# Performance work log

Hardware: AMD Instinct MI355X
Metric: run time of the kernel (lower is better)

Reference implementation:

```python
import jax, jax.numpy as jnp
import numpy as np

L, D, H, T, B, V, R = 12, 1024, 16, 1024, 2, 50257, 32
HD = D // H
LORA_SCALE = 64.0 / 32.0  # alpha / rank
EPS = 1e-5


def setup_inputs() -> dict:
    key = jax.random.key(0)
    ks = iter(jax.random.split(key, 32))
    f = lambda shape, s=0.02: jax.random.normal(next(ks), shape, dtype=jnp.float32) * s
    inp = {
        'input_ids': jax.random.randint(next(ks), (B, T), 0, V, dtype=jnp.int64),
        'wte': f((V, D)), 'wpe': f((T, D)),
        'ln1_w': jnp.ones((L, D), jnp.float32), 'ln1_b': jnp.zeros((L, D), jnp.float32),
        'attn_w': f((L, 3 * D, D)), 'attn_b': jnp.zeros((L, 3 * D), jnp.float32),
        'attn_la': f((L, R, D), 0.01), 'attn_lb': f((L, 3 * D, R), 0.01),
        'proj_w': f((L, D, D)), 'proj_b': jnp.zeros((L, D), jnp.float32),
        'proj_la': f((L, R, D), 0.01), 'proj_lb': f((L, D, R), 0.01),
        'ln2_w': jnp.ones((L, D), jnp.float32), 'ln2_b': jnp.zeros((L, D), jnp.float32),
        'fc_w': f((L, 4 * D, D)), 'fc_b': jnp.zeros((L, 4 * D), jnp.float32),
        'fc_la': f((L, R, D), 0.01), 'fc_lb': f((L, 4 * D, R), 0.01),
        'mp_w': f((L, D, 4 * D)), 'mp_b': jnp.zeros((L, D), jnp.float32),
        'mp_la': f((L, R, 4 * D), 0.01), 'mp_lb': f((L, D, R), 0.01),
        'lnf_w': jnp.ones((D,), jnp.float32), 'lnf_b': jnp.zeros((D,), jnp.float32),
    }
    return inp


def _ln(x, w, b):
    m = jnp.mean(x, axis=-1, keepdims=True)
    v = jnp.mean(jnp.square(x - m), axis=-1, keepdims=True)
    return (x - m) * jax.lax.rsqrt(v + EPS) * w + b


def _lin(x, W, b, A, Bm):
    # quantized linear at 32-bit (pass-through) + LoRA: x W^T + b + scale * (x A^T) B^T
    return x @ W.T + b + ((x @ A.T) @ Bm.T) * LORA_SCALE


def _forward(input_ids, wte, wpe, ln1_w, ln1_b, attn_w, attn_b, attn_la, attn_lb,
             proj_w, proj_b, proj_la, proj_lb, ln2_w, ln2_b, fc_w, fc_b, fc_la, fc_lb,
             mp_w, mp_b, mp_la, mp_lb, lnf_w, lnf_b):
    Bq, Tq = input_ids.shape
    mask = jnp.tril(jnp.ones((Tq, Tq), dtype=bool))  # causal bias buffer
    h = wte[input_ids] + wpe[jnp.arange(Tq)]  # embed + (eval-mode) dropout

    def blk(h, p):
        l1w, l1b, aw, ab, ala, alb, pw, pb, pla, plb, l2w, l2b, fw, fb, fla, flb, mw, mb, mla, mlb = p
        x = _ln(h, l1w, l1b)
        qkv = _lin(x, aw, ab, ala, alb)  # [B,T,3D]
        q, k, v = jnp.split(qkv, 3, axis=-1)
        q = q.reshape(Bq, Tq, H, HD).transpose(0, 2, 1, 3)
        k = k.reshape(Bq, Tq, H, HD).transpose(0, 2, 1, 3)
        v = v.reshape(Bq, Tq, H, HD).transpose(0, 2, 1, 3)
        s = jnp.einsum('bhqd,bhkd->bhqk', q, k) / jnp.sqrt(jnp.float32(HD))
        s = jnp.where(mask, s, -jnp.inf)
        pa = jax.nn.softmax(s, axis=-1)
        o = jnp.einsum('bhqk,bhkd->bhqd', pa, v).transpose(0, 2, 1, 3).reshape(Bq, Tq, D)
        h = h + _lin(o, pw, pb, pla, plb)
        x = _ln(h, l2w, l2b)
        m = jax.nn.gelu(_lin(x, fw, fb, fla, flb), approximate=False)
        h = h + _lin(m, mw, mb, mla, mlb)
        return h, None

    h, _ = jax.lax.scan(blk, h, (ln1_w, ln1_b, attn_w, attn_b, attn_la, attn_lb,
                                 proj_w, proj_b, proj_la, proj_lb, ln2_w, ln2_b,
                                 fc_w, fc_b, fc_la, fc_lb, mp_w, mp_b, mp_la, mp_lb))
    return _ln(h, lnf_w, lnf_b)


def reference(input_ids, wte, wpe, ln1_w, ln1_b, attn_w, attn_b, attn_la, attn_lb,
              proj_w, proj_b, proj_la, proj_lb, ln2_w, ln2_b, fc_w, fc_b, fc_la, fc_lb,
              mp_w, mp_b, mp_la, mp_lb, lnf_w, lnf_b):
    return _forward(input_ids, wte, wpe, ln1_w, ln1_b, attn_w, attn_b, attn_la, attn_lb,
                    proj_w, proj_b, proj_la, proj_lb, ln2_w, ln2_b, fc_w, fc_b, fc_la, fc_lb,
                    mp_w, mp_b, mp_la, mp_lb, lnf_w, lnf_b)
```

## Files before the change

### kernel.cpp

```cpp
#include <hip/hip_runtime.h>
#include <math.h>

#define TT 1024
#define DD 1024
#define NH 16
#define NB 2
#define NL 12
#define RR 32
#define MM (NB * TT)

typedef __attribute__((ext_vector_type(8))) short bf16x8;
typedef __attribute__((ext_vector_type(4))) float f32x4;

__device__ __forceinline__ unsigned short f2bf(float f) {
  unsigned int u = __float_as_uint(f);
  u = (u + 0x7FFFu + ((u >> 16) & 1u)) >> 16;
  return (unsigned short)u;
}
__device__ __forceinline__ float bf2f(unsigned short u) {
  return __uint_as_float((unsigned int)u << 16);
}

typedef __attribute__((address_space(1))) void gvoid;
typedef __attribute__((address_space(3))) void lvoid;
__device__ __forceinline__ void gload_lds16(const void* g, void* l) {
  __builtin_amdgcn_global_load_lds((gvoid*)g, (lvoid*)l, 16, 0, 0);
}

__global__ __launch_bounds__(256) void embed_cvt_k(
    const int* __restrict__ ids, const float* __restrict__ wte,
    const float* __restrict__ wpe, float* __restrict__ h,
    const float* __restrict__ ala, const float* __restrict__ alb,
    const float* __restrict__ pla, const float* __restrict__ plb,
    const float* __restrict__ fla, const float* __restrict__ flb,
    const float* __restrict__ mla, const float* __restrict__ mlb,
    unsigned short* __restrict__ out) {
  if (blockIdx.x < MM * DD / 256) {
    const int i = blockIdx.x * 256 + threadIdx.x;
    const int row = i >> 10;
    const int d = i & 1023;
    const int t = row & (TT - 1);
    const int id = ids[row];
    h[i] = wte[(size_t)id * DD + d] + wpe[(size_t)t * DD + d];
    return;
  }
  const int g = (blockIdx.x - MM * DD / 256) * 256 + threadIdx.x;
  const int layer = g >> 19;
  const int rem = g & 524287;
  const int row = rem >> 5;
  const int r = rem & 31;
  float v;
  if (row < 1024)       v = ala[(size_t)layer * 32 * 1024 + r * 1024 + row];
  else if (row < 4096)  v = alb[(size_t)layer * 3072 * 32 + (row - 1024) * 32 + r];
  else if (row < 5120)  v = pla[(size_t)layer * 32 * 1024 + r * 1024 + (row - 4096)];
  else if (row < 6144)  v = plb[(size_t)layer * 1024 * 32 + (row - 5120) * 32 + r];
  else if (row < 7168)  v = fla[(size_t)layer * 32 * 1024 + r * 1024 + (row - 6144)];
  else if (row < 11264) v = flb[(size_t)layer * 4096 * 32 + (row - 7168) * 32 + r];
  else if (row < 15360) v = mla[(size_t)layer * 32 * 4096 + r * 4096 + (row - 11264)];
  else                  v = mlb[(size_t)layer * 1024 * 32 + (row - 15360) * 32 + r];
  out[g] = f2bf(v);
}

__global__ __launch_bounds__(256) void ln_bf_k(const float* __restrict__ x,
                                               const float* __restrict__ w,
                                               const float* __restrict__ b,
                                               unsigned short* __restrict__ out) {
  const int row = blockIdx.x;
  const float* xr = x + (size_t)row * DD;
  const float4 v = *(const float4*)(xr + threadIdx.x * 4);
  float s = v.x + v.y + v.z + v.w;
  float ss = v.x * v.x + v.y * v.y + v.z * v.z + v.w * v.w;
#pragma unroll
  for (int off = 32; off > 0; off >>= 1) {
    s += __shfl_down(s, off);
    ss += __shfl_down(ss, off);
  }
  __shared__ float rs[4], rss[4];
  const int wid = threadIdx.x >> 6;
  if ((threadIdx.x & 63) == 0) { rs[wid] = s; rss[wid] = ss; }
  __syncthreads();
  s = rs[0] + rs[1] + rs[2] + rs[3];
  ss = rss[0] + rss[1] + rss[2] + rss[3];
  const float mean = s * (1.f / DD);
  const float var = ss * (1.f / DD) - mean * mean;
  const float rstd = rsqrtf(var + 1e-5f);
  const float4 wv = *(const float4*)(w + threadIdx.x * 4);
  const float4 bv = *(const float4*)(b + threadIdx.x * 4);
  ushort4 o;
  o.x = f2bf((v.x - mean) * rstd * wv.x + bv.x);
  o.y = f2bf((v.y - mean) * rstd * wv.y + bv.y);
  o.z = f2bf((v.z - mean) * rstd * wv.z + bv.z);
  o.w = f2bf((v.w - mean) * rstd * wv.w + bv.w);
  *(ushort4*)(out + (size_t)row * DD + threadIdx.x * 4) = o;
}

__global__ __launch_bounds__(256) void ln_f_k(const float* __restrict__ x,
                                              const float* __restrict__ w,
                                              const float* __restrict__ b,
                                              float* __restrict__ out) {
  const int row = blockIdx.x;
  const float* xr = x + (size_t)row * DD;
  const float4 v = *(const float4*)(xr + threadIdx.x * 4);
  float s = v.x + v.y + v.z + v.w;
  float ss = v.x * v.x + v.y * v.y + v.z * v.z + v.w * v.w;
#pragma unroll
  for (int off = 32; off > 0; off >>= 1) {
    s += __shfl_down(s, off);
    ss += __shfl_down(ss, off);
  }
  __shared__ float rs[4], rss[4];
  const int wid = threadIdx.x >> 6;
  if ((threadIdx.x & 63) == 0) { rs[wid] = s; rss[wid] = ss; }
  __syncthreads();
  s = rs[0] + rs[1] + rs[2] + rs[3];
  ss = rss[4 - 4] + rss[1] + rss[2] + rss[3];
  const float mean = s * (1.f / DD);
  const float var = ss * (1.f / DD) - mean * mean;
  const float rstd = rsqrtf(var + 1e-5f);
  const float4 wv = *(const float4*)(w + threadIdx.x * 4);
  const float4 bv = *(const float4*)(b + threadIdx.x * 4);
  float4 o;
  o.x = (v.x - mean) * rstd * wv.x + bv.x;
  o.y = (v.y - mean) * rstd * wv.y + bv.y;
  o.z = (v.z - mean) * rstd * wv.z + bv.z;
  o.w = (v.w - mean) * rstd * wv.w + bv.w;
  *(float4*)(out + (size_t)row * DD + threadIdx.x * 4) = o;
}

__global__ __launch_bounds__(256) void fold_ln_k(
    const float* __restrict__ aw, const float* __restrict__ pw,
    const float* __restrict__ fw, const float* __restrict__ mw,
    const unsigned short* __restrict__ Lb,
    unsigned short* __restrict__ oq, unsigned short* __restrict__ op_,
    unsigned short* __restrict__ of, unsigned short* __restrict__ om,
    const float* __restrict__ hln, const float* __restrict__ lnw,
    const float* __restrict__ lnb, unsigned short* __restrict__ xout) {
  __shared__ unsigned short dl[64 * 128];
  const int tid = threadIdx.x;
  if (blockIdx.x >= 1536) {
    const int row = blockIdx.x - 1536;
    const float* xr = hln + (size_t)row * DD;
    const float4 v = *(const float4*)(xr + tid * 4);
    float s = v.x + v.y + v.z + v.w;
    float ss = v.x * v.x + v.y * v.y + v.z * v.z + v.w * v.w;
#pragma unroll
    for (int off = 32; off > 0; off >>= 1) {
      s += __shfl_down(s, off);
      ss += __shfl_down(ss, off);
    }
    float* red = (float*)dl;
    const int wid = tid >> 6;
    if ((tid & 63) == 0) { red[wid] = s; red[4 + wid] = ss; }
    __syncthreads();
    s = red[0] + red[1] + red[2] + red[3];
    ss = red[4] + red[5] + red[6] + red[7];
    const float mean = s * (1.f / DD);
    const float var = ss * (1.f / DD) - mean * mean;
    const float rstd = rsqrtf(var + 1e-5f);
    const float4 wv = *(const float4*)(lnw + tid * 4);
    const float4 bv = *(const float4*)(lnb + tid * 4);
    ushort4 o;
    o.x = f2bf((v.x - mean) * rstd * wv.x + bv.x);
    o.y = f2bf((v.y - mean) * rstd * wv.y + bv.y);
    o.z = f2bf((v.z - mean) * rstd * wv.z + bv.z);
    o.w = f2bf((v.w - mean) * rstd * wv.w + bv.w);
    *(ushort4*)(xout + (size_t)row * DD + tid * 4) = o;
    return;
  }
  const int lid = blockIdx.x;
  const float* W;
  unsigned short* out;
  const unsigned short *Bl, *Al;
  int K, n0, kblk;
  if (lid < 384) {
    W = aw; out = oq; Bl = Lb + 1024 * 32; Al = Lb;
    K = DD; n0 = (lid >> 3) * 64; kblk = (lid & 7) * 128;
  } else if (lid < 512) {
    const int t = lid - 384;
    W = pw; out = op_; Bl = Lb + 5120 * 32; Al = Lb + 4096 * 32;
    K = DD; n0 = (t >> 3) * 64; kblk = (t & 7) * 128;
  } else if (lid < 1024) {
    const int t = lid - 512;
    W = fw; out = of; Bl = Lb + 7168 * 32; Al = Lb + 6144 * 32;
    K = DD; n0 = (t >> 3) * 64; kblk = (t & 7) * 128;
  } else {
    const int t = lid - 1024;
    W = mw; out = om; Bl = Lb + 15360 * 32; Al = Lb + 11264 * 32;
    K = 4 * DD; n0 = (t >> 5) * 64; kblk = (t & 31) * 128;
  }
  const int w = tid >> 6, l = tid & 63;
  const int lr16 = l & 15, lg = l >> 4;
  const int nloc = w * 16 + lr16;
  const bf16x8 bfrag = *(const bf16x8*)(Bl + (size_t)(n0 + nloc) * 32 + lg * 8);
#pragma unroll
  for (int kc = 0; kc < 8; ++kc) {
    const bf16x8 afr = *(const bf16x8*)(Al + (size_t)(kblk + kc * 16 + lr16) * 32 + lg * 8);
    f32x4 acc = {};
    acc = __builtin_amdgcn_mfma_f32_16x16x32_bf16(afr, bfrag, acc, 0, 0, 0);
    ushort4 dv;
    dv.x = f2bf(2.f * acc[0]); dv.y = f2bf(2.f * acc[1]);
    dv.z = f2bf(2.f * acc[2]); dv.w = f2bf(2.f * acc[3]);
    const unsigned int byte = ((unsigned)(nloc * 256 + kc * 32 + lg * 8)) ^
                              (((unsigned)nloc & 3u) << 5);
    *(ushort4*)((char*)dl + byte) = dv;
  }
  __syncthreads();
  float4 wv[8];
#pragma unroll
  for (int it = 0; it < 8; ++it) {
    const int flat = it * 1024 + tid * 4;
    const int row = flat >> 7;
    const int k = flat & 127;
    wv[it] = *(const float4*)(W + (size_t)(n0 + row) * K + kblk + k);
  }
  asm volatile("s_waitcnt vmcnt(0)" ::: "memory");
#pragma unroll
  for (int it = 0; it < 8; ++it) {
    const int flat = it * 1024 + tid * 4;
    const int row = flat >> 7;
    const int k = flat & 127;
    const unsigned int byte = ((unsigned)(row * 256 + k * 2)) ^
                              (((unsigned)row & 3u) << 5);
    const ushort4 dv = *(const ushort4*)((const char*)dl + byte);
    ushort4 o;
    o.x = f2bf(wv[it].x + bf2f(dv.x));
    o.y = f2bf(wv[it].y + bf2f(dv.y));
    o.z = f2bf(wv[it].z + bf2f(dv.z));
    o.w = f2bf(wv[it].w + bf2f(dv.w));
    *(ushort4*)(out + (size_t)(n0 + row) * K + kblk + k) = o;
  }
}

template <int BMt, int BNt, int BKt, int MODE>
__global__ __launch_bounds__(256) void gemm_t(const unsigned short* __restrict__ A,
                                              const unsigned short* __restrict__ Wt,
                                              const float* __restrict__ bias,
                                              const float* __restrict__ res,
                                              float* __restrict__ Cf,
                                              unsigned short* __restrict__ Cb,
                                              unsigned short* __restrict__ vt,
                                              int M, int N, int K) {
  constexpr int MI2 = BMt / 32, NJ2 = BNt / 32;
  constexpr int SB = BKt * 2;
  constexpr int SL = BKt / 8;
  constexpr int RC = 1024 / SB;
  constexpr int CAw = BMt / RC / 4;
  constexpr int CBw = BNt / RC / 4;
  __shared__ unsigned short As[BMt * BKt];
  __shared__ unsigned short Bs[BNt * BKt];
  const int tid = threadIdx.x;
  const int w = tid >> 6, l = tid & 63;
  const int gx = gridDim.x;
  const int bid = blockIdx.y * gx + blockIdx.x;
  const int cpx = (gx * gridDim.y) >> 3;
  const int logical = (bid & 7) * cpx + (bid >> 3);
  const int bm = (logical / gx) * BMt, bn = (logical % gx) * BNt;
  const int wr = w >> 1, wc = w & 1;
  const int lr16 = l & 15, lg = l >> 4, l7 = l & 7;
  const int rin = l / SL;
  const int slot = l % SL;
  f32x4 acc[MI2][NJ2] = {};
  for (int k0 = 0; k0 < K; k0 += BKt) {
    __syncthreads();
#pragma unroll
    for (int i = 0; i < CAw; ++i) {
      const int ch = w * CAw + i;
      const int row = ch * RC + rin;
      gload_lds16(A + (size_t)(bm + row) * K + k0 + ((slot ^ (row & 7)) * 8),
                  (char*)As + ch * 1024);
    }
#pragma unroll
    for (int i = 0; i < CBw; ++i) {
      const int ch = w * CBw + i;
      const int row = ch * RC + rin;
      gload_lds16(Wt + (size_t)(bn + row) * K + k0 + ((slot ^ (row & 7)) * 8),
                  (char*)Bs + ch * 1024);
    }
    __syncthreads();
#pragma unroll
    for (int kk = 0; kk < BKt / 32; ++kk) {
      bf16x8 af[MI2], bfr[NJ2];
      const int q = (kk * 4 + lg) ^ l7;
#pragma unroll
      for (int mi = 0; mi < MI2; ++mi)
        af[mi] = *(const bf16x8*)((const char*)As +
            (wr * (BMt / 2) + mi * 16 + lr16) * SB + q * 16);
#pragma unroll
      for (int nj = 0; nj < NJ2; ++nj)
        bfr[nj] = *(const bf16x8*)((const char*)Bs +
            (wc * (BNt / 2) + nj * 16 + lr16) * SB + q * 16);
#pragma unroll
      for (int mi = 0; mi < MI2; ++mi)
#pragma unroll
        for (int nj = 0; nj < NJ2; ++nj)
          acc[mi][nj] = __builtin_amdgcn_mfma_f32_16x16x32_bf16(
              af[mi], bfr[nj], acc[mi][nj], 0, 0, 0);
    }
  }
  const int cr = lg * 4;
  const int cc = lr16;
#pragma unroll
  for (int mi = 0; mi < MI2; ++mi) {
    const int gr0 = bm + wr * (BMt / 2) + mi * 16 + cr;
#pragma unroll
    for (int nj = 0; nj < NJ2; ++nj) {
      const int gc = bn + wc * (BNt / 2) + nj * 16 + cc;
      const float bv = bias[gc];
      if (MODE == 3) {
        if (gc < 2048) {
#pragma unroll
          for (int r = 0; r < 4; ++r)
            Cb[(size_t)(gr0 + r) * 2048 + gc] = f2bf(acc[mi][nj][r] + bv);
        } else {
          const int hv = gc - 2048;
          const int b_ = gr0 >> 10, t0 = gr0 & 1023;
          ushort4 u;
          u.x = f2bf(acc[mi][nj][0] + bv); u.y = f2bf(acc[mi][nj][1] + bv);
          u.z = f2bf(acc[mi][nj][2] + bv); u.w = f2bf(acc[mi][nj][3] + bv);
          *(ushort4*)(vt + ((size_t)(b_ * 1024 + hv)) * 1024 + t0) = u;
        }
      } else if (MODE == 1) {
#pragma unroll
        for (int r = 0; r < 4; ++r) {
          const size_t idx = (size_t)(gr0 + r) * N + gc;
          Cf[idx] = acc[mi][nj][r] + bv + res[idx];
        }
      } else {
#pragma unroll
        for (int r = 0; r < 4; ++r) {
          float v = acc[mi][nj][r] + bv;
          v = 0.5f * v * (1.f + erff(v * 0.70710678118654752f));
          Cb[(size_t)(gr0 + r) * N + gc] = f2bf(v);
        }
      }
    }
  }
}

#define SM_SCALE_LOG2E 0.18033688011112042f
__global__ __launch_bounds__(256) void attn4_k(const unsigned short* __restrict__ qk,
                                               const unsigned short* __restrict__ vt,
                                               unsigned short* __restrict__ out) {
  const int qt = 15 - blockIdx.x;
  const int bh = blockIdx.y;
  const int b = bh >> 4, hh = bh & 15;
  const int tid = threadIdx.x;
  const int w = tid >> 6, l = tid & 63;
  const int lg = l >> 4;
  const int lr = l & 15;

  __shared__ unsigned short Kt[2][128 * 64];
  __shared__ unsigned short Vb[2][64 * 128];
  __shared__ unsigned short Pb[4][16 * 128];

  bf16x8 qf[2];
  {
    const unsigned short* qp =
        qk + ((size_t)(b * TT + qt * 64 + w * 16 + lr)) * 2048 + hh * 64 + lg * 8;
    qf[0] = *(const bf16x8*)(qp);
    qf[1] = *(const bf16x8*)(qp + 32);
  }
  f32x4 oacc[4] = {};
  float mrow[4] = {-1e30f, -1e30f, -1e30f, -1e30f};
  float lrow[4] = {0.f, 0.f, 0.f, 0.f};

  auto stage = [&](int buf, int kt2) {
#pragma unroll
    for (int i = 0; i < 4; ++i) {
      const int ch = w * 4 + i;
      const int row = ch * 8 + (l >> 3);
      const int sc = ((l & 7) ^ (l >> 3)) * 8;
      const unsigned short* ks =
          qk + ((size_t)(b * TT + kt2 * 128 + row)) * 2048 + 1024 + hh * 64 + sc;
      gload_lds16(ks, (char*)&Kt[buf][0] + ch * 1024);
    }
#pragma unroll
    for (int i = 0; i < 4; ++i) {
      const int ch = w * 4 + i;
      const int row = ch * 4 + (l >> 4);
      const int sc = ((l & 15) ^ (row & 15)) * 8;
      const unsigned short* vs =
          vt + ((size_t)(bh * 64 + row)) * 1024 + kt2 * 128 + sc;
      gload_lds16(vs, (char*)&Vb[buf][0] + ch * 1024);
    }
  };

  const int nkt = (qt >> 1) + 1;
  stage(0, 0);
  int cur = 0;
  unsigned short* Pw = &Pb[w][0];
  const int qlocal = w * 16 + lg * 4;

  for (int kt2 = 0; kt2 < nkt; ++kt2) {
    __syncthreads();
    if (kt2 + 1 < nkt) stage(cur ^ 1, kt2 + 1);
    const unsigned short* Kb_ = &Kt[cur][0];
    const unsigned short* Vb_ = &Vb[cur][0];
    const bool last = (kt2 == nkt - 1);

    f32x4 s[8];
    __builtin_amdgcn_s_setprio(1);
#pragma unroll
    for (int j = 0; j < 8; ++j) {
      f32x4 sj = {};
#pragma unroll
      for (int ks = 0; ks < 2; ++ks) {
        const bf16x8 kf = *(const bf16x8*)((const char*)Kb_ + (j * 16 + lr) * 128 +
                                           (((ks * 4 + lg) ^ (lr & 7)) * 16));
        sj = __builtin_amdgcn_mfma_f32_16x16x32_bf16(qf[ks], kf, sj, 0, 0, 0);
      }
      s[j] = sj;
    }
    __builtin_amdgcn_s_setprio(0);

#pragma unroll
    for (int j = 0; j < 8; ++j)
#pragma unroll
      for (int r = 0; r < 4; ++r) {
        float v = s[j][r] * SM_SCALE_LOG2E;
        if (last && (kt2 * 128 + j * 16 + lr > qt * 64 + qlocal + r)) v = -1e30f;
        s[j][r] = v;
      }
    float corr[4];
#pragma unroll
    for (int r = 0; r < 4; ++r) {
      float mx = s[0][r];
#pragma unroll
      for (int j = 1; j < 8; ++j) mx = fmaxf(mx, s[j][r]);
      mx = fmaxf(mx, __shfl_xor(mx, 1));
      mx = fmaxf(mx, __shfl_xor(mx, 2));
      mx = fmaxf(mx, __shfl_xor(mx, 4));
      mx = fmaxf(mx, __shfl_xor(mx, 8));
      const float mn = fmaxf(mrow[r], mx);
      corr[r] = exp2f(mrow[r] - mn);
      mrow[r] = mn;
      lrow[r] *= corr[r];
    }
#pragma unroll
    for (int dt = 0; dt < 4; ++dt) {
      oacc[dt][0] *= corr[0]; oacc[dt][1] *= corr[1];
      oacc[dt][2] *= corr[2]; oacc[dt][3] *= corr[3];
    }
#pragma unroll
    for (int j = 0; j < 8; ++j)
#pragma unroll
      for (int r = 0; r < 4; ++r) {
        const float p = exp2f(s[j][r] - mrow[r]);
        lrow[r] += p;
        const int q = lg * 4 + r;
        const int kv = j * 16 + lr;
        *(unsigned short*)((char*)Pw + q * 256 + ((kv * 2) ^ ((q & 15) << 4))) = f2bf(p);
      }
    asm volatile("s_waitcnt lgkmcnt(0)" ::: "memory");
    __builtin_amdgcn_sched_barrier(0);

    __builtin_amdgcn_s_setprio(1);
#pragma unroll
    for (int ks = 0; ks < 4; ++ks) {
      const bf16x8 pf = *(const bf16x8*)((const char*)Pw + lr * 256 +
                                         (((ks * 4 + lg) ^ (lr & 15)) * 16));
#pragma unroll
      for (int dt = 0; dt < 4; ++dt) {
        const bf16x8 vf = *(const bf16x8*)((const char*)Vb_ + (dt * 16 + lr) * 256 +
                                           (((ks * 4 + lg) ^ (lr & 15)) * 16));
        oacc[dt] = __builtin_amdgcn_mfma_f32_16x16x32_bf16(pf, vf, oacc[dt], 0, 0, 0);
      }
    }
    __builtin_amdgcn_s_setprio(0);
    cur ^= 1;
  }

#pragma unroll
  for (int r = 0; r < 4; ++r) {
    float lv = lrow[r];
    lv += __shfl_xor(lv, 1);
    lv += __shfl_xor(lv, 2);
    lv += __shfl_xor(lv, 4);
    lv += __shfl_xor(lv, 8);
    lrow[r] = 1.f / lv;
  }
  unsigned short* ob = out + ((size_t)(b * TT + qt * 64 + w * 16 + lg * 4)) * 1024 + hh * 64 + lr;
#pragma unroll
  for (int r = 0; r < 4; ++r)
#pragma unroll
    for (int dt = 0; dt < 4; ++dt)
      ob[(size_t)r * 1024 + dt * 16] = f2bf(oacc[dt][r] * lrow[r]);
}

extern "C" void kernel_launch(void* const* d_in, const int* in_sizes, int n_in,
                              void* d_out, int out_size, void* d_ws, size_t ws_size,
                              hipStream_t stream) {
  (void)in_sizes; (void)n_in; (void)out_size; (void)ws_size;
  const int* ids = (const int*)d_in[0];
  const float* wte = (const float*)d_in[1];
  const float* wpe = (const float*)d_in[2];
  const float* ln1w = (const float*)d_in[3];
  const float* ln1b = (const float*)d_in[4];
  const float* attnw = (const float*)d_in[5];
  const float* attnb = (const float*)d_in[6];
  const float* attnla = (const float*)d_in[7];
  const float* attnlb = (const float*)d_in[8];
  const float* projw = (const float*)d_in[9];
  const float* projb = (const float*)d_in[10];
  const float* projla = (const float*)d_in[11];
  const float* projlb = (const float*)d_in[12];
  const float* ln2w = (const float*)d_in[13];
  const float* ln2b = (const float*)d_in[14];
  const float* fcw = (const float*)d_in[15];
  const float* fcb = (const float*)d_in[16];
  const float* fcla = (const float*)d_in[17];
  const float* fclb = (const float*)d_in[18];
  const float* mpw = (const float*)d_in[19];
  const float* mpb = (const float*)d_in[20];
  const float* mpla = (const float*)d_in[21];
  const float* mplb = (const float*)d_in[22];
  const float* lnfw = (const float*)d_in[23];
  const float* lnfb = (const float*)d_in[24];

  char* ws = (char*)d_ws;
  float* h = (float*)ws;                        ws += (size_t)MM * DD * 4;
  unsigned short* x = (unsigned short*)ws;      ws += (size_t)MM * DD * 2;
  unsigned short* qkb = (unsigned short*)ws;    ws += (size_t)MM * 2 * DD * 2;
  unsigned short* vtb = (unsigned short*)ws;    ws += (size_t)MM * DD * 2;
  unsigned short* ho = (unsigned short*)ws;     ws += (size_t)MM * DD * 2;
  unsigned short* hm = (unsigned short*)ws;     ws += (size_t)MM * 4 * DD * 2;
  unsigned short* wqkv = (unsigned short*)ws;   ws += (size_t)3 * DD * DD * 2;
  unsigned short* wproj = (unsigned short*)ws;  ws += (size_t)DD * DD * 2;
  unsigned short* wfc = (unsigned short*)ws;    ws += (size_t)4 * DD * DD * 2;
  unsigned short* wmp = (unsigned short*)ws;    ws += (size_t)DD * 4 * DD * 2;
  unsigned short* loraP = (unsigned short*)ws;  ws += (size_t)NL * 16384 * 32 * 2;

  hipLaunchKernelGGL(embed_cvt_k, dim3(MM * DD / 256 + NL * 16384 * 32 / 256), dim3(256),
                     0, stream, ids, wte, wpe, h,
                     attnla, attnlb, projla, projlb, fcla, fclb, mpla, mplb, loraP);

  for (int l = 0; l < NL; ++l) {
    const float* ab = attnb + (size_t)l * 3 * DD;
    const float* pb = projb + (size_t)l * DD;
    const float* fb = fcb + (size_t)l * 4 * DD;
    const float* mb = mpb + (size_t)l * DD;

    hipLaunchKernelGGL(fold_ln_k, dim3(1536 + MM), dim3(256), 0, stream,
                       attnw + (size_t)l * 3 * DD * DD, projw + (size_t)l * DD * DD,
                       fcw + (size_t)l * 4 * DD * DD, mpw + (size_t)l * DD * 4 * DD,
                       loraP + (size_t)l * 16384 * 32, wqkv, wproj, wfc, wmp,
                       h, ln1w + (size_t)l * DD, ln1b + (size_t)l * DD, x);

    hipLaunchKernelGGL((gemm_t<128, 64, 128, 3>), dim3(3 * DD / 64, MM / 128), dim3(256), 0,
                       stream, x, wqkv, ab, (const float*)nullptr, (float*)nullptr,
                       qkb, vtb, MM, 3 * DD, DD);
    hipLaunchKernelGGL(attn4_k, dim3(TT / 64, NB * NH), dim3(256), 0, stream, qkb, vtb, ho);
    hipLaunchKernelGGL((gemm_t<64, 64, 256, 1>), dim3(DD / 64, MM / 64), dim3(256), 0,
                       stream, ho, wproj, pb, h, h, (unsigned short*)nullptr,
                       (unsigned short*)nullptr, MM, DD, DD);
    hipLaunchKernelGGL(ln_bf_k, dim3(MM), dim3(256), 0, stream, h,
                       ln2w + (size_t)l * DD, ln2b + (size_t)l * DD, x);
    hipLaunchKernelGGL((gemm_t<128, 128, 128, 2>), dim3(4 * DD / 128, MM / 128), dim3(256), 0,
                       stream, x, wfc, fb, (const float*)nullptr, (float*)nullptr, hm,
                       (unsigned short*)nullptr, MM, 4 * DD, DD);
    hipLaunchKernelGGL((gemm_t<64, 64, 256, 1>), dim3(DD / 64, MM / 64), dim3(256), 0,
                       stream, hm, wmp, mb, h, h, (unsigned short*)nullptr,
                       (unsigned short*)nullptr, MM, DD, 4 * DD);
  }

  hipLaunchKernelGGL(ln_f_k, dim3(MM), dim3(256), 0, stream, h, lnfw, lnfb, (float*)d_out);
}
```

Measured before the change: 1.742 ms.

## Overlap next layer's LoRA weight folding with the FC GEMM via double buffers

Moves the per-layer LoRA-fold of the next layer's weights out of the layer-start fold+LN kernel and into a combined kernel that also runs the FC GEMM. Extra blocks handle the fold, and the folded weights go into double-buffered workspaces. Layers after the first then only run a plain LayerNorm before the QKV GEMM. This is meant to hide the memory-bound fold traffic behind the compute-bound FC GEMM. In exchange it doubles the folded-weight workspace, and the fold blocks compete with GEMM blocks for CUs and LDS.

```diff
diff --git a/kernel.cpp b/kernel.cpp
--- a/kernel.cpp
+++ b/kernel.cpp
@@ -113,7 +113,7 @@
   if ((threadIdx.x & 63) == 0) { rs[wid] = s; rss[wid] = ss; }
   __syncthreads();
   s = rs[0] + rs[1] + rs[2] + rs[3];
-  ss = rss[4 - 4] + rss[1] + rss[2] + rss[3];
+  ss = rss[0] + rss[1] + rss[2] + rss[3];
   const float mean = s * (1.f / DD);
   const float var = ss * (1.f / DD) - mean * mean;
   const float rstd = rsqrtf(var + 1e-5f);
@@ -127,47 +127,13 @@
   *(float4*)(out + (size_t)row * DD + threadIdx.x * 4) = o;
 }
 
-__global__ __launch_bounds__(256) void fold_ln_k(
+__device__ __forceinline__ void fold_body(
+    int lid, char* smem,
     const float* __restrict__ aw, const float* __restrict__ pw,
     const float* __restrict__ fw, const float* __restrict__ mw,
     const unsigned short* __restrict__ Lb,
     unsigned short* __restrict__ oq, unsigned short* __restrict__ op_,
-    unsigned short* __restrict__ of, unsigned short* __restrict__ om,
-    const float* __restrict__ hln, const float* __restrict__ lnw,
-    const float* __restrict__ lnb, unsigned short* __restrict__ xout) {
-  __shared__ unsigned short dl[64 * 128];
-  const int tid = threadIdx.x;
-  if (blockIdx.x >= 1536) {
-    const int row = blockIdx.x - 1536;
-    const float* xr = hln + (size_t)row * DD;
-    const float4 v = *(const float4*)(xr + tid * 4);
-    float s = v.x + v.y + v.z + v.w;
-    float ss = v.x * v.x + v.y * v.y + v.z * v.z + v.w * v.w;
-#pragma unroll
-    for (int off = 32; off > 0; off >>= 1) {
-      s += __shfl_down(s, off);
-      ss += __shfl_down(ss, off);
-    }
-    float* red = (float*)dl;
-    const int wid = tid >> 6;
-    if ((tid & 63) == 0) { red[wid] = s; red[4 + wid] = ss; }
-    __syncthreads();
-    s = red[0] + red[1] + red[2] + red[3];
-    ss = red[4] + red[5] + red[6] + red[7];
-    const float mean = s * (1.f / DD);
-    const float var = ss * (1.f / DD) - mean * mean;
-    const float rstd = rsqrtf(var + 1e-5f);
-    const float4 wv = *(const float4*)(lnw + tid * 4);
-    const float4 bv = *(const float4*)(lnb + tid * 4);
-    ushort4 o;
-    o.x = f2bf((v.x - mean) * rstd * wv.x + bv.x);
-    o.y = f2bf((v.y - mean) * rstd * wv.y + bv.y);
-    o.z = f2bf((v.z - mean) * rstd * wv.z + bv.z);
-    o.w = f2bf((v.w - mean) * rstd * wv.w + bv.w);
-    *(ushort4*)(xout + (size_t)row * DD + tid * 4) = o;
-    return;
-  }
-  const int lid = blockIdx.x;
+    unsigned short* __restrict__ of, unsigned short* __restrict__ om) {
   const float* W;
   unsigned short* out;
   const unsigned short *Bl, *Al;
@@ -188,6 +154,8 @@
     W = mw; out = om; Bl = Lb + 15360 * 32; Al = Lb + 11264 * 32;
     K = 4 * DD; n0 = (t >> 5) * 64; kblk = (t & 31) * 128;
   }
+  unsigned short* dl = (unsigned short*)smem;
+  const int tid = threadIdx.x;
   const int w = tid >> 6, l = tid & 63;
   const int lr16 = l & 15, lg = l >> 4;
   const int nloc = w * 16 + lr16;
@@ -229,6 +197,49 @@
     o.w = f2bf(wv[it].w + bf2f(dv.w));
     *(ushort4*)(out + (size_t)(n0 + row) * K + kblk + k) = o;
   }
+}
+
+__global__ __launch_bounds__(256) void fold_ln_k(
+    const float* __restrict__ aw, const float* __restrict__ pw,
+    const float* __restrict__ fw, const float* __restrict__ mw,
+    const unsigned short* __restrict__ Lb,
+    unsigned short* __restrict__ oq, unsigned short* __restrict__ op_,
+    unsigned short* __restrict__ of, unsigned short* __restrict__ om,
+    const float* __restrict__ hln, const float* __restrict__ lnw,
+    const float* __restrict__ lnb, unsigned short* __restrict__ xout) {
+  __shared__ char smem[64 * 128 * 2];
+  const int tid = threadIdx.x;
+  if (blockIdx.x >= 1536) {
+    const int row = blockIdx.x - 1536;
+    const float* xr = hln + (size_t)row * DD;
+    const float4 v = *(const float4*)(xr + tid * 4);
+    float s = v.x + v.y + v.z + v.w;
+    float ss = v.x * v.x + v.y * v.y + v.z * v.z + v.w * v.w;
+#pragma unroll
+    for (int off = 32; off > 0; off >>= 1) {
+      s += __shfl_down(s, off);
+      ss += __shfl_down(ss, off);
+    }
+    float* red = (float*)smem;
+    const int wid = tid >> 6;
+    if ((tid & 63) == 0) { red[wid] = s; red[4 + wid] = ss; }
+    __syncthreads();
+    s = red[0] + red[1] + red[2] + red[3];
+    ss = red[4] + red[5] + red[6] + red[7];
+    const float mean = s * (1.f / DD);
+    const float var = ss * (1.f / DD) - mean * mean;
+    const float rstd = rsqrtf(var + 1e-5f);
+    const float4 wv = *(const float4*)(lnw + tid * 4);
+    const float4 bv = *(const float4*)(lnb + tid * 4);
+    ushort4 o;
+    o.x = f2bf((v.x - mean) * rstd * wv.x + bv.x);
+    o.y = f2bf((v.y - mean) * rstd * wv.y + bv.y);
+    o.z = f2bf((v.z - mean) * rstd * wv.z + bv.z);
+    o.w = f2bf((v.w - mean) * rstd * wv.w + bv.w);
+    *(ushort4*)(xout + (size_t)row * DD + tid * 4) = o;
+    return;
+  }
+  fold_body(blockIdx.x, smem, aw, pw, fw, mw, Lb, oq, op_, of, om);
 }
 
 template <int BMt, int BNt, int BKt, int MODE>
@@ -337,6 +348,86 @@
   }
 }
 
+__global__ __launch_bounds__(256) void gemm_fc_fold_k(
+    const unsigned short* __restrict__ A, const unsigned short* __restrict__ Wt,
+    const float* __restrict__ bias, unsigned short* __restrict__ Cb,
+    const float* __restrict__ aw, const float* __restrict__ pw,
+    const float* __restrict__ fw, const float* __restrict__ mw,
+    const unsigned short* __restrict__ Lb,
+    unsigned short* __restrict__ oq, unsigned short* __restrict__ op_,
+    unsigned short* __restrict__ of, unsigned short* __restrict__ om) {
+  __shared__ char smem[128 * 128 * 2 * 2];
+  const int tid = threadIdx.x;
+  if (blockIdx.x >= 512) {
+    fold_body(blockIdx.x - 512, smem, aw, pw, fw, mw, Lb, oq, op_, of, om);
+    return;
+  }
+  constexpr int N = 4096, K = 1024;
+  unsigned short* As = (unsigned short*)smem;
+  unsigned short* Bs = (unsigned short*)(smem + 128 * 128 * 2);
+  const int w = tid >> 6, l = tid & 63;
+  const int bid = blockIdx.x;
+  const int logical = (bid & 7) * 64 + (bid >> 3);
+  const int bm = (logical >> 5) * 128, bn = (logical & 31) * 128;
+  const int wr = w >> 1, wc = w & 1;
+  const int lr16 = l & 15, lg = l >> 4, l7 = l & 7;
+  const int rin = l / 16;
+  const int slot = l % 16;
+  f32x4 acc[4][4] = {};
+  for (int k0 = 0; k0 < K; k0 += 128) {
+    __syncthreads();
+#pragma unroll
+    for (int i = 0; i < 8; ++i) {
+      const int ch = w * 8 + i;
+      const int row = ch * 4 + rin;
+      gload_lds16(A + (size_t)(bm + row) * K + k0 + ((slot ^ (row & 7)) * 8),
+                  (char*)As + ch * 1024);
+    }
+#pragma unroll
+    for (int i = 0; i < 8; ++i) {
+      const int ch = w * 8 + i;
+      const int row = ch * 4 + rin;
+      gload_lds16(Wt + (size_t)(bn + row) * K + k0 + ((slot ^ (row & 7)) * 8),
+                  (char*)Bs + ch * 1024);
+    }
+    __syncthreads();
+#pragma unroll
+    for (int kk = 0; kk < 4; ++kk) {
+      bf16x8 af[4], bfr[4];
+      const int q = (kk * 4 + lg) ^ l7;
+#pragma unroll
+      for (int mi = 0; mi < 4; ++mi)
+        af[mi] = *(const bf16x8*)((const char*)As + (wr * 64 + mi * 16 + lr16) * 256 + q * 16);
+#pragma unroll
+      for (int nj = 0; nj < 4; ++nj)
+        bfr[nj] = *(const bf16x8*)((const char*)Bs + (wc * 64 + nj * 16 + lr16) * 256 + q * 16);
+#pragma unroll
+      for (int mi = 0; mi < 4; ++mi)
+#pragma unroll
+        for (int nj = 0; nj < 4; ++nj)
+          acc[mi][nj] = __builtin_amdgcn_mfma_f32_16x16x32_bf16(
+              af[mi], bfr[nj], acc[mi][nj], 0, 0, 0);
+    }
+  }
+  const int cr = lg * 4;
+  const int cc = lr16;
+#pragma unroll
+  for (int mi = 0; mi < 4; ++mi) {
+    const int gr0 = bm + wr * 64 + mi * 16 + cr;
+#pragma unroll
+    for (int nj = 0; nj < 4; ++nj) {
+      const int gc = bn + wc * 64 + nj * 16 + cc;
+      const float bv = bias[gc];
+#pragma unroll
+      for (int r = 0; r < 4; ++r) {
+        float v = acc[mi][nj][r] + bv;
+        v = 0.5f * v * (1.f + erff(v * 0.70710678118654752f));
+        Cb[(size_t)(gr0 + r) * N + gc] = f2bf(v);
+      }
+    }
+  }
+}
+
 #define SM_SCALE_LOG2E 0.18033688011112042f
 __global__ __launch_bounds__(256) void attn4_k(const unsigned short* __restrict__ qk,
                                                const unsigned short* __restrict__ vt,
@@ -524,10 +615,13 @@
   unsigned short* vtb = (unsigned short*)ws;    ws += (size_t)MM * DD * 2;
   unsigned short* ho = (unsigned short*)ws;     ws += (size_t)MM * DD * 2;
   unsigned short* hm = (unsigned short*)ws;     ws += (size_t)MM * 4 * DD * 2;
-  unsigned short* wqkv = (unsigned short*)ws;   ws += (size_t)3 * DD * DD * 2;
-  unsigned short* wproj = (unsigned short*)ws;  ws += (size_t)DD * DD * 2;
-  unsigned short* wfc = (unsigned short*)ws;    ws += (size_t)4 * DD * DD * 2;
-  unsigned short* wmp = (unsigned short*)ws;    ws += (size_t)DD * 4 * DD * 2;
+  unsigned short* wqkvB[2], *wprojB[2], *wfcB[2], *wmpB[2];
+  for (int p = 0; p < 2; ++p) {
+    wqkvB[p] = (unsigned short*)ws; ws += (size_t)3 * DD * DD * 2;
+    wprojB[p] = (unsigned short*)ws; ws += (size_t)DD * DD * 2;
+    wfcB[p] = (unsigned short*)ws;  ws += (size_t)4 * DD * DD * 2;
+    wmpB[p] = (unsigned short*)ws;  ws += (size_t)DD * 4 * DD * 2;
+  }
   unsigned short* loraP = (unsigned short*)ws;  ws += (size_t)NL * 16384 * 32 * 2;
 
   hipLaunchKernelGGL(embed_cvt_k, dim3(MM * DD / 256 + NL * 16384 * 32 / 256), dim3(256),
@@ -535,31 +629,49 @@
                      attnla, attnlb, projla, projlb, fcla, fclb, mpla, mplb, loraP);
 
   for (int l = 0; l < NL; ++l) {
+    const int p = l & 1, pn = (l + 1) & 1;
     const float* ab = attnb + (size_t)l * 3 * DD;
     const float* pb = projb + (size_t)l * DD;
     const float* fb = fcb + (size_t)l * 4 * DD;
     const float* mb = mpb + (size_t)l * DD;
 
-    hipLaunchKernelGGL(fold_ln_k, dim3(1536 + MM), dim3(256), 0, stream,
-                       attnw + (size_t)l * 3 * DD * DD, projw + (size_t)l * DD * DD,
-                       fcw + (size_t)l * 4 * DD * DD, mpw + (size_t)l * DD * 4 * DD,
-                       loraP + (size_t)l * 16384 * 32, wqkv, wproj, wfc, wmp,
-                       h, ln1w + (size_t)l * DD, ln1b + (size_t)l * DD, x);
+    if (l == 0) {
+      hipLaunchKernelGGL(fold_ln_k, dim3(1536 + MM), dim3(256), 0, stream,
+                         attnw, projw, fcw, mpw, loraP,
+                         wqkvB[0], wprojB[0], wfcB[0], wmpB[0],
+                         h, ln1w, ln1b, x);
+    } else {
+      hipLaunchKernelGGL(ln_bf_k, dim3(MM), dim3(256), 0, stream, h,
+                         ln1w + (size_t)l * DD, ln1b + (size_t)l * DD, x);
+    }
 
     hipLaunchKernelGGL((gemm_t<128, 64, 128, 3>), dim3(3 * DD / 64, MM / 128), dim3(256), 0,
-                       stream, x, wqkv, ab, (const float*)nullptr, (float*)nullptr,
+                       stream, x, wqkvB[p], ab, (const float*)nullptr, (float*)nullptr,
                        qkb, vtb, MM, 3 * DD, DD);
     hipLaunchKernelGGL(attn4_k, dim3(TT / 64, NB * NH), dim3(256), 0, stream, qkb, vtb, ho);
     hipLaunchKernelGGL((gemm_t<64, 64, 256, 1>), dim3(DD / 64, MM / 64), dim3(256), 0,
-                       stream, ho, wproj, pb, h, h, (unsigned short*)nullptr,
+                       stream, ho, wprojB[p], pb, h, h, (unsigned short*)nullptr,
                        (unsigned short*)nullptr, MM, DD, DD);
     hipLaunchKernelGGL(ln_bf_k, dim3(MM), dim3(256), 0, stream, h,
                        ln2w + (size_t)l * DD, ln2b + (size_t)l * DD, x);
-    hipLaunchKernelGGL((gemm_t<128, 128, 128, 2>), dim3(4 * DD / 128, MM / 128), dim3(256), 0,
-                       stream, x, wfc, fb, (const float*)nullptr, (float*)nullptr, hm,
-                       (unsigned short*)nullptr, MM, 4 * DD, DD);
+
+    if (l + 1 < NL) {
+      hipLaunchKernelGGL(gemm_fc_fold_k, dim3(512 + 1536), dim3(256), 0, stream,
+                         x, wfcB[p], fb, hm,
+                         attnw + (size_t)(l + 1) * 3 * DD * DD,
+                         projw + (size_t)(l + 1) * DD * DD,
+                         fcw + (size_t)(l + 1) * 4 * DD * DD,
+                         mpw + (size_t)(l + 1) * DD * 4 * DD,
+                         loraP + (size_t)(l + 1) * 16384 * 32,
+                         wqkvB[pn], wprojB[pn], wfcB[pn], wmpB[pn]);
+    } else {
+      hipLaunchKernelGGL((gemm_t<128, 128, 128, 2>), dim3(4 * DD / 128, MM / 128), dim3(256),
+                         0, stream, x, wfcB[p], fb, (const float*)nullptr, (float*)nullptr,
+                         hm, (unsigned short*)nullptr, MM, 4 * DD, DD);
+    }
+
     hipLaunchKernelGGL((gemm_t<64, 64, 256, 1>), dim3(DD / 64, MM / 64), dim3(256), 0,
-                       stream, hm, wmp, mb, h, h, (unsigned short*)nullptr,
+                       stream, hm, wmpB[p], mb, h, h, (unsigned short*)nullptr,
                        (unsigned short*)nullptr, MM, DD, 4 * DD);
   }
 
```

New measurement: 1.791 ms. 1.03x slower.
